# Optimization experiments

Hardware: AMD Instinct MI355X
Metric: run time of the kernel (lower is better)

Reference implementation:

```python
import jax, jax.numpy as jnp
import numpy as np

N_NODES = 100000
N_EDGES = 3200000
N_GRAPHS = 1024


def _glorot(key, shape):
    fan_in, fan_out = shape[0], shape[1]
    lim = jnp.sqrt(6.0 / (fan_in + fan_out))
    return jax.random.uniform(key, shape, minval=-lim, maxval=lim, dtype=jnp.float32)


def setup_inputs() -> dict:
    key = jax.random.key(0)
    ks = jax.random.split(key, 9)
    x = jax.random.normal(ks[0], (N_NODES, 3), dtype=jnp.float32)
    edge_index = jax.random.randint(ks[1], (2, N_EDGES), 0, N_NODES, dtype=jnp.int64)
    batch = jnp.sort(jax.random.randint(ks[2], (N_NODES,), 0, N_GRAPHS, dtype=jnp.int64))
    return {
        "x": x,
        "edge_index": edge_index,
        "batch": batch,
        "W1": _glorot(ks[3], (3, 16)),
        "b1": jnp.zeros((16,), jnp.float32),
        "W2": _glorot(ks[4], (16, 16)),
        "b2": jnp.zeros((16,), jnp.float32),
        "Wl": _glorot(ks[5], (16, 7)),
        "bl": jnp.zeros((7,), jnp.float32),
    }


def gcn_conv(x, edge_index, W, b, num_nodes):
    """GCNConv with normalize=True, add_self_loops=True (PyG defaults)."""
    x = x @ W  # linear transform first: [N, F_out]
    loop = jnp.arange(num_nodes, dtype=edge_index.dtype)
    row = jnp.concatenate([edge_index[0], loop])  # source nodes
    col = jnp.concatenate([edge_index[1], loop])  # target nodes
    # degree of target nodes (edge weight 1 incl. self loops)
    deg = jax.ops.segment_sum(jnp.ones_like(col, dtype=x.dtype), col,
                              num_segments=num_nodes)
    dinv = jnp.where(deg > 0, jax.lax.rsqrt(deg), 0.0)
    norm = dinv[row] * dinv[col]  # [E+N]
    msg = x[row] * norm[:, None]  # gather + normalize
    out = jax.ops.segment_sum(msg, col, num_segments=num_nodes)  # scatter-add
    return out + b


def reference(x, edge_index, batch, W1, b1, W2, b2, Wl, bl):
    h = jax.nn.relu(gcn_conv(x, edge_index, W1, b1, N_NODES))
    h = gcn_conv(h, edge_index, W2, b2, N_NODES)
    pooled = jax.ops.segment_sum(h, batch, num_segments=N_GRAPHS)  # global_add_pool
    logits = pooled @ Wl + bl  # [G, 7]
    return jax.nn.log_softmax(logits, axis=1)
```

## Files before the change

### kernel.cpp

```cpp
#include <hip/hip_runtime.h>
#include <hip/hip_fp16.h>
#include <math.h>

#define N_NODES  100000
#define N_EDGES  3200000
#define N_GRAPHS 1024
#define NB_NODE  391
#define NBUCK    391
#define CAP      8960
#define NPS      512
#define ECH      6250

__device__ inline unsigned pack2(float a, float b) {
    union { __half2 h; unsigned u; } c;
    c.h = __floats2half2_rn(a, b);
    return c.u;
}
__device__ inline float2 up2(unsigned u) {
    union { unsigned u; __half2 h; } c; c.u = u;
    return __half22float2(c.h);
}
__device__ inline void acc8(float* a, uint4 v) {
    float2 f;
    f = up2(v.x); a[0] += f.x; a[1] += f.y;
    f = up2(v.y); a[2] += f.x; a[3] += f.y;
    f = up2(v.z); a[4] += f.x; a[5] += f.y;
    f = up2(v.w); a[6] += f.x; a[7] += f.y;
}

__global__ void k_initcur(int* __restrict__ gcursor) {
    int t = blockIdx.x * blockDim.x + threadIdx.x;
    if (t < NBUCK) gcursor[t] = t * CAP;
}

__global__ void k_pair_scatter(const int* __restrict__ row, const int* __restrict__ col,
                               int* __restrict__ gcursor, int* __restrict__ pairbuf) {
    __shared__ int            sbuf[ECH];
    __shared__ unsigned short sbk[ECH];
    __shared__ int            lhist[NBUCK];
    __shared__ int            lcur[NBUCK];
    __shared__ int            wbase[NBUCK];
    int t = threadIdx.x;
    int e0 = blockIdx.x * ECH;
    int n = N_EDGES - e0; if (n > ECH) n = ECH;
    for (int j = t; j < NBUCK; j += 256) lhist[j] = 0;
    __syncthreads();
    for (int k = t; k < n; k += 256)
        atomicAdd(&lhist[col[e0 + k] >> 8], 1);
    __syncthreads();
    if (t < 64) {
        int carry = 0;
        for (int c0 = 0; c0 < NBUCK; c0 += 64) {
            int idx = c0 + t;
            int v = (idx < NBUCK) ? lhist[idx] : 0;
            int orig = v;
#pragma unroll
            for (int o = 1; o < 64; o <<= 1) {
                int u = __shfl_up(v, o, 64);
                if (t >= o) v += u;
            }
            if (idx < NBUCK) lcur[idx] = v - orig + carry;
            carry += __shfl(v, 63, 64);
        }
    }
    __syncthreads();
    for (int j = t; j < NBUCK; j += 256) {
        int c = lhist[j];
        int g = c ? atomicAdd(&gcursor[j], c) : 0;
        wbase[j] = g - lcur[j];
    }
    __syncthreads();
    for (int k = t; k < n; k += 256) {
        int e = e0 + k;
        int c = col[e];
        int bk = c >> 8;
        int pos = atomicAdd(&lcur[bk], 1);
        sbuf[pos] = row[e] | ((c & 255) << 17);
        sbk[pos] = (unsigned short)bk;
    }
    __syncthreads();
    for (int k = t; k < n; k += 256) {
        int bk = sbk[k];
        int pos = wbase[bk] + k;
        if (pos < (bk + 1) * CAP)
            pairbuf[pos] = sbuf[k];
    }
}

__global__ void k_finalize(const int* __restrict__ pairbuf, const int* __restrict__ gcursor,
                           int2* __restrict__ rowse, float* __restrict__ dinv,
                           int* __restrict__ csr) {
    __shared__ int slice[CAP];
    __shared__ int lcnt[256];
    __shared__ int ls[256];
    __shared__ int cur[256];
    int t = threadIdx.x, b = blockIdx.x;
    int base = b * CAP;
    int cnt_b = gcursor[b] - base;
    if (cnt_b > CAP) cnt_b = CAP;
    lcnt[t] = 0;
    for (int k = t; k < cnt_b; k += 256) slice[k] = pairbuf[base + k];
    __syncthreads();
    for (int k = t; k < cnt_b; k += 256)
        atomicAdd(&lcnt[(slice[k] >> 17) & 255], 1);
    __syncthreads();
    int myc = lcnt[t];
    ls[t] = myc;
    __syncthreads();
    for (int o = 1; o < 256; o <<= 1) {
        int v = (t >= o) ? ls[t - o] : 0;
        __syncthreads();
        ls[t] += v;
        __syncthreads();
    }
    int node0 = b << 8;
    int nn = N_NODES - node0; if (nn > 256) nn = 256;
    int st = base + ls[t] - myc;
    cur[t] = st;
    if (t < nn) {
        rowse[node0 + t] = make_int2(st, st + myc);
        dinv[node0 + t] = rsqrtf((float)(myc + 1));
    }
    __syncthreads();
    for (int k = t; k < cnt_b; k += 256) {
        int p = slice[k];
        int pos = atomicAdd(&cur[(p >> 17) & 255], 1);
        csr[pos] = p & 0x1FFFF;
    }
}

__global__ void k_xw1(const float* __restrict__ dinv, const float* __restrict__ x,
                      const float* __restrict__ W1, __half* __restrict__ bufA16) {
    int i = blockIdx.x * blockDim.x + threadIdx.x;
    if (i >= N_NODES) return;
    float d = dinv[i];
    float x0 = x[i * 3 + 0], x1 = x[i * 3 + 1], x2 = x[i * 3 + 2];
    float v[16];
#pragma unroll
    for (int j = 0; j < 16; j++)
        v[j] = (x0 * W1[j] + x1 * W1[16 + j] + x2 * W1[32 + j]) * d;
    uint4 u0 = { pack2(v[0], v[1]), pack2(v[2], v[3]), pack2(v[4], v[5]), pack2(v[6], v[7]) };
    uint4 u1 = { pack2(v[8], v[9]), pack2(v[10], v[11]), pack2(v[12], v[13]), pack2(v[14], v[15]) };
    uint4* p = (uint4*)(bufA16 + (long long)i * 16);
    p[0] = u0; p[1] = u1;
}

__global__ void k_gather(const uint4* __restrict__ src16, const int* __restrict__ csr,
                         const int2* __restrict__ rowse, const float* __restrict__ dinv,
                         float* __restrict__ dst) {
    int t = threadIdx.x;
    int node = blockIdx.x * 128 + (t >> 1);
    int h = t & 1;
    if (node >= N_NODES) return;
    int2 se = rowse[node];
    int s = se.x, e = se.y;
    float acc[8];
    {
        uint4 u = src16[node * 2 + h];
        float2 f;
        f = up2(u.x); acc[0] = f.x; acc[1] = f.y;
        f = up2(u.y); acc[2] = f.x; acc[3] = f.y;
        f = up2(u.z); acc[4] = f.x; acc[5] = f.y;
        f = up2(u.w); acc[6] = f.x; acc[7] = f.y;
    }
    int j = s;
    for (; j + 8 <= e; j += 8) {
        int i0 = csr[j],     i1 = csr[j + 1], i2 = csr[j + 2], i3 = csr[j + 3];
        int i4 = csr[j + 4], i5 = csr[j + 5], i6 = csr[j + 6], i7 = csr[j + 7];
        uint4 v0 = src16[i0 * 2 + h], v1 = src16[i1 * 2 + h];
        uint4 v2 = src16[i2 * 2 + h], v3 = src16[i3 * 2 + h];
        uint4 v4 = src16[i4 * 2 + h], v5 = src16[i5 * 2 + h];
        uint4 v6 = src16[i6 * 2 + h], v7 = src16[i7 * 2 + h];
        acc8(acc, v0); acc8(acc, v1); acc8(acc, v2); acc8(acc, v3);
        acc8(acc, v4); acc8(acc, v5); acc8(acc, v6); acc8(acc, v7);
    }
    for (; j < e; j++) {
        int si = csr[j];
        acc8(acc, src16[si * 2 + h]);
    }
    float d = dinv[node];
    float4 o0 = { acc[0] * d, acc[1] * d, acc[2] * d, acc[3] * d };
    float4 o1 = { acc[4] * d, acc[5] * d, acc[6] * d, acc[7] * d };
    float4* dp = (float4*)(dst + (long long)node * 16 + h * 8);
    dp[0] = o0; dp[1] = o1;
}

__global__ void k_layer2(const float* __restrict__ b1, const float* __restrict__ W2,
                         const float* __restrict__ dinv,
                         __half* __restrict__ bufA16, const float* __restrict__ bufB) {
    __shared__ float sW[256];
    __shared__ float sB[16];
    int tid = threadIdx.x;
    if (tid < 256) sW[tid] = W2[tid];
    if (tid < 16) sB[tid] = b1[tid];
    __syncthreads();
    int i = blockIdx.x * blockDim.x + tid;
    if (i >= N_NODES) return;
    float hbuf[16];
#pragma unroll
    for (int k = 0; k < 16; k++) {
        float v = bufB[i * 16 + k] + sB[k];
        hbuf[k] = v > 0.f ? v : 0.f;
    }
    float d = dinv[i];
    float v[16];
#pragma unroll
    for (int j = 0; j < 16; j++) {
        float acc = 0.f;
#pragma unroll
        for (int k = 0; k < 16; k++) acc += hbuf[k] * sW[k * 16 + j];
        v[j] = acc * d;
    }
    uint4 u0 = { pack2(v[0], v[1]), pack2(v[2], v[3]), pack2(v[4], v[5]), pack2(v[6], v[7]) };
    uint4 u1 = { pack2(v[8], v[9]), pack2(v[10], v[11]), pack2(v[12], v[13]), pack2(v[14], v[15]) };
    uint4* p = (uint4*)(bufA16 + (long long)i * 16);
    p[0] = u0; p[1] = u1;
}

__global__ void k_pool_head(const float* __restrict__ agg2, const int* __restrict__ batch,
                            const float* __restrict__ b2, const float* __restrict__ Wl,
                            const float* __restrict__ bl, float* __restrict__ out) {
    int g = blockIdx.x;
    int t = threadIdx.x;
    __shared__ int range[2];
    __shared__ float part[64];
    __shared__ float pooled[16];
    __shared__ float logits[7];
    if (t < 2) {
        int target = g + t;
        int lo = 0, hi = N_NODES;
        while (lo < hi) {
            int mid = (lo + hi) >> 1;
            if (batch[mid] < target) lo = mid + 1; else hi = mid;
        }
        range[t] = lo;
    }
    __syncthreads();
    int s = range[0], e = range[1];
    int f = t & 15, chunk = t >> 4;
    float acc = 0.f;
    for (int i = s + chunk; i < e; i += 4) acc += agg2[(long long)i * 16 + f];
    part[t] = acc;
    __syncthreads();
    if (t < 16) {
        float p = part[t] + part[t + 16] + part[t + 32] + part[t + 48];
        pooled[t] = p + (float)(e - s) * b2[t];
    }
    __syncthreads();
    if (t < 7) {
        float a = bl[t];
#pragma unroll
        for (int k = 0; k < 16; k++) a += pooled[k] * Wl[k * 7 + t];
        logits[t] = a;
    }
    __syncthreads();
    if (t == 0) {
        float m = logits[0];
#pragma unroll
        for (int c = 1; c < 7; c++) m = fmaxf(m, logits[c]);
        float sum = 0.f;
#pragma unroll
        for (int c = 0; c < 7; c++) sum += expf(logits[c] - m);
        float lse = logf(sum) + m;
#pragma unroll
        for (int c = 0; c < 7; c++) out[g * 7 + c] = logits[c] - lse;
    }
}

extern "C" void kernel_launch(void* const* d_in, const int* in_sizes, int n_in,
                              void* d_out, int out_size, void* d_ws, size_t ws_size,
                              hipStream_t stream) {
    const float* x     = (const float*)d_in[0];
    const int*   ei    = (const int*)d_in[1];
    const int*   batch = (const int*)d_in[2];
    const float* W1    = (const float*)d_in[3];
    const float* b1    = (const float*)d_in[4];
    const float* W2    = (const float*)d_in[5];
    const float* b2    = (const float*)d_in[6];
    const float* Wl    = (const float*)d_in[7];
    const float* bl    = (const float*)d_in[8];
    float* out = (float*)d_out;

    const int* row = ei;
    const int* col = ei + N_EDGES;

    int*    gcursor = (int*)d_ws;
    float*  dinv    = (float*)d_ws + 400;
    int2*   rowse   = (int2*)((int*)d_ws + 100400);
    int*    csr     = (int*)d_ws + 300400;
    int*    pairbuf = (int*)d_ws + 3803760;
    __half* bufA16  = (__half*)pairbuf;
    float*  bufB    = (float*)pairbuf + 800000;

    const int BT = 256;
    int gatherBlocks = (N_NODES + 127) / 128;

    k_initcur<<<2, BT, 0, stream>>>(gcursor);
    k_pair_scatter<<<NPS, BT, 0, stream>>>(row, col, gcursor, pairbuf);
    k_finalize<<<NBUCK, BT, 0, stream>>>(pairbuf, gcursor, rowse, dinv, csr);
    k_xw1<<<NB_NODE, BT, 0, stream>>>(dinv, x, W1, bufA16);
    k_gather<<<gatherBlocks, BT, 0, stream>>>((const uint4*)bufA16, csr, rowse, dinv, bufB);
    k_layer2<<<NB_NODE, BT, 0, stream>>>(b1, W2, dinv, bufA16, bufB);
    k_gather<<<gatherBlocks, BT, 0, stream>>>((const uint4*)bufA16, csr, rowse, dinv, bufB);
    k_pool_head<<<N_GRAPHS, 64, 0, stream>>>(bufB, batch, b2, Wl, bl, out);
}
```

Baseline: 233.2 us.

## Fuse XW1 into CSR finalize and layer-2 transform into first gather

The first-layer linear transform moves into the CSR finalize kernel, and the bias/ReLU/W2 transform moves into the first gather kernel through shared memory. This removes two launches and the fp32 intermediate round trip through global memory. The second gather now uses four threads per node with uint2 loads, and the CSR is written in place into the pair buffer. Cursor init becomes a memset, and the scatter uses more, smaller chunks without bounds checks. The fused gather adds a block-level sync and extra shared memory per block.

```diff
diff --git a/kernel.cpp b/kernel.cpp
--- a/kernel.cpp
+++ b/kernel.cpp
@@ -5,11 +5,10 @@
 #define N_NODES  100000
 #define N_EDGES  3200000
 #define N_GRAPHS 1024
-#define NB_NODE  391
 #define NBUCK    391
 #define CAP      8960
-#define NPS      512
-#define ECH      6250
+#define NPS      1024
+#define ECH      3125
 
 __device__ inline unsigned pack2(float a, float b) {
     union { __half2 h; unsigned u; } c;
@@ -27,10 +26,10 @@
     f = up2(v.z); a[4] += f.x; a[5] += f.y;
     f = up2(v.w); a[6] += f.x; a[7] += f.y;
 }
-
-__global__ void k_initcur(int* __restrict__ gcursor) {
-    int t = blockIdx.x * blockDim.x + threadIdx.x;
-    if (t < NBUCK) gcursor[t] = t * CAP;
+__device__ inline void acc4(float* a, uint2 v) {
+    float2 f;
+    f = up2(v.x); a[0] += f.x; a[1] += f.y;
+    f = up2(v.y); a[2] += f.x; a[3] += f.y;
 }
 
 __global__ void k_pair_scatter(const int* __restrict__ row, const int* __restrict__ col,
@@ -42,10 +41,9 @@
     __shared__ int            wbase[NBUCK];
     int t = threadIdx.x;
     int e0 = blockIdx.x * ECH;
-    int n = N_EDGES - e0; if (n > ECH) n = ECH;
     for (int j = t; j < NBUCK; j += 256) lhist[j] = 0;
     __syncthreads();
-    for (int k = t; k < n; k += 256)
+    for (int k = t; k < ECH; k += 256)
         atomicAdd(&lhist[col[e0 + k] >> 8], 1);
     __syncthreads();
     if (t < 64) {
@@ -67,10 +65,10 @@
     for (int j = t; j < NBUCK; j += 256) {
         int c = lhist[j];
         int g = c ? atomicAdd(&gcursor[j], c) : 0;
-        wbase[j] = g - lcur[j];
-    }
-    __syncthreads();
-    for (int k = t; k < n; k += 256) {
+        wbase[j] = j * CAP + g - lcur[j];
+    }
+    __syncthreads();
+    for (int k = t; k < ECH; k += 256) {
         int e = e0 + k;
         int c = col[e];
         int bk = c >> 8;
@@ -79,7 +77,7 @@
         sbk[pos] = (unsigned short)bk;
     }
     __syncthreads();
-    for (int k = t; k < n; k += 256) {
+    for (int k = t; k < ECH; k += 256) {
         int bk = sbk[k];
         int pos = wbase[bk] + k;
         if (pos < (bk + 1) * CAP)
@@ -87,18 +85,21 @@
     }
 }
 
-__global__ void k_finalize(const int* __restrict__ pairbuf, const int* __restrict__ gcursor,
+__global__ void k_finalize(int* __restrict__ pairbuf, const int* __restrict__ gcursor,
                            int2* __restrict__ rowse, float* __restrict__ dinv,
-                           int* __restrict__ csr) {
+                           const float* __restrict__ x, const float* __restrict__ W1,
+                           __half* __restrict__ bufA16) {
     __shared__ int slice[CAP];
     __shared__ int lcnt[256];
     __shared__ int ls[256];
     __shared__ int cur[256];
+    __shared__ float sw1[48];
     int t = threadIdx.x, b = blockIdx.x;
     int base = b * CAP;
-    int cnt_b = gcursor[b] - base;
+    int cnt_b = gcursor[b];
     if (cnt_b > CAP) cnt_b = CAP;
     lcnt[t] = 0;
+    if (t < 48) sw1[t] = W1[t];
     for (int k = t; k < cnt_b; k += 256) slice[k] = pairbuf[base + k];
     __syncthreads();
     for (int k = t; k < cnt_b; k += 256)
@@ -113,49 +114,48 @@
         ls[t] += v;
         __syncthreads();
     }
-    int node0 = b << 8;
-    int nn = N_NODES - node0; if (nn > 256) nn = 256;
+    int node = (b << 8) + t;
     int st = base + ls[t] - myc;
     cur[t] = st;
-    if (t < nn) {
-        rowse[node0 + t] = make_int2(st, st + myc);
-        dinv[node0 + t] = rsqrtf((float)(myc + 1));
+    if (node < N_NODES) {
+        rowse[node] = make_int2(st, st + myc);
+        float d = rsqrtf((float)(myc + 1));
+        dinv[node] = d;
+        float x0 = x[node * 3 + 0], x1 = x[node * 3 + 1], x2 = x[node * 3 + 2];
+        float v[16];
+#pragma unroll
+        for (int j = 0; j < 16; j++)
+            v[j] = (x0 * sw1[j] + x1 * sw1[16 + j] + x2 * sw1[32 + j]) * d;
+        uint4 u0 = { pack2(v[0], v[1]), pack2(v[2], v[3]), pack2(v[4], v[5]), pack2(v[6], v[7]) };
+        uint4 u1 = { pack2(v[8], v[9]), pack2(v[10], v[11]), pack2(v[12], v[13]), pack2(v[14], v[15]) };
+        uint4* p = (uint4*)(bufA16 + (long long)node * 16);
+        p[0] = u0; p[1] = u1;
     }
     __syncthreads();
     for (int k = t; k < cnt_b; k += 256) {
         int p = slice[k];
         int pos = atomicAdd(&cur[(p >> 17) & 255], 1);
-        csr[pos] = p & 0x1FFFF;
-    }
-}
-
-__global__ void k_xw1(const float* __restrict__ dinv, const float* __restrict__ x,
-                      const float* __restrict__ W1, __half* __restrict__ bufA16) {
-    int i = blockIdx.x * blockDim.x + threadIdx.x;
-    if (i >= N_NODES) return;
-    float d = dinv[i];
-    float x0 = x[i * 3 + 0], x1 = x[i * 3 + 1], x2 = x[i * 3 + 2];
-    float v[16];
-#pragma unroll
-    for (int j = 0; j < 16; j++)
-        v[j] = (x0 * W1[j] + x1 * W1[16 + j] + x2 * W1[32 + j]) * d;
-    uint4 u0 = { pack2(v[0], v[1]), pack2(v[2], v[3]), pack2(v[4], v[5]), pack2(v[6], v[7]) };
-    uint4 u1 = { pack2(v[8], v[9]), pack2(v[10], v[11]), pack2(v[12], v[13]), pack2(v[14], v[15]) };
-    uint4* p = (uint4*)(bufA16 + (long long)i * 16);
-    p[0] = u0; p[1] = u1;
-}
-
-__global__ void k_gather(const uint4* __restrict__ src16, const int* __restrict__ csr,
-                         const int2* __restrict__ rowse, const float* __restrict__ dinv,
-                         float* __restrict__ dst) {
+        pairbuf[pos] = p & 0x1FFFF;
+    }
+}
+
+__global__ void k_gather1(const uint4* __restrict__ src16, const int* __restrict__ csr,
+                          const int2* __restrict__ rowse, const float* __restrict__ dinv,
+                          const float* __restrict__ b1, const float* __restrict__ W2,
+                          __half* __restrict__ out16) {
+    __shared__ float sh[128][17];
+    __shared__ float sW[256];
+    __shared__ float sb1[16];
     int t = threadIdx.x;
-    int node = blockIdx.x * 128 + (t >> 1);
-    int h = t & 1;
-    if (node >= N_NODES) return;
-    int2 se = rowse[node];
+    sW[t] = W2[t];
+    if (t < 16) sb1[t] = b1[t];
+    int local = t >> 1, h = t & 1;
+    int node = blockIdx.x * 128 + local;
+    bool act = node < N_NODES;
+    int2 se = act ? rowse[node] : make_int2(0, 0);
     int s = se.x, e = se.y;
-    float acc[8];
-    {
+    float acc[8] = {0, 0, 0, 0, 0, 0, 0, 0};
+    if (act) {
         uint4 u = src16[node * 2 + h];
         float2 f;
         f = up2(u.x); acc[0] = f.x; acc[1] = f.y;
@@ -174,47 +174,60 @@
         acc8(acc, v0); acc8(acc, v1); acc8(acc, v2); acc8(acc, v3);
         acc8(acc, v4); acc8(acc, v5); acc8(acc, v6); acc8(acc, v7);
     }
-    for (; j < e; j++) {
-        int si = csr[j];
-        acc8(acc, src16[si * 2 + h]);
-    }
+    for (; j < e; j++) acc8(acc, src16[csr[j] * 2 + h]);
+    float d = act ? dinv[node] : 0.f;
+#pragma unroll
+    for (int k = 0; k < 8; k++) {
+        float v = acc[k] * d + sb1[h * 8 + k];
+        sh[local][h * 8 + k] = v > 0.f ? v : 0.f;
+    }
+    __syncthreads();
+    float v[8];
+#pragma unroll
+    for (int jj = 0; jj < 8; jj++) {
+        int jo = h * 8 + jj;
+        float a = 0.f;
+#pragma unroll
+        for (int k = 0; k < 16; k++) a += sh[local][k] * sW[k * 16 + jo];
+        v[jj] = a * d;
+    }
+    if (act) {
+        uint4 u = { pack2(v[0], v[1]), pack2(v[2], v[3]), pack2(v[4], v[5]), pack2(v[6], v[7]) };
+        ((uint4*)(out16 + (long long)node * 16 + h * 8))[0] = u;
+    }
+}
+
+__global__ void k_gather2(const uint2* __restrict__ src16, const int* __restrict__ csr,
+                          const int2* __restrict__ rowse, const float* __restrict__ dinv,
+                          float* __restrict__ dst) {
+    int t = threadIdx.x;
+    int node = blockIdx.x * 64 + (t >> 2);
+    int h = t & 3;
+    if (node >= N_NODES) return;
+    int2 se = rowse[node];
+    int s = se.x, e = se.y;
+    float acc[4];
+    {
+        uint2 u = src16[node * 4 + h];
+        float2 f;
+        f = up2(u.x); acc[0] = f.x; acc[1] = f.y;
+        f = up2(u.y); acc[2] = f.x; acc[3] = f.y;
+    }
+    int j = s;
+    for (; j + 8 <= e; j += 8) {
+        int i0 = csr[j],     i1 = csr[j + 1], i2 = csr[j + 2], i3 = csr[j + 3];
+        int i4 = csr[j + 4], i5 = csr[j + 5], i6 = csr[j + 6], i7 = csr[j + 7];
+        uint2 v0 = src16[i0 * 4 + h], v1 = src16[i1 * 4 + h];
+        uint2 v2 = src16[i2 * 4 + h], v3 = src16[i3 * 4 + h];
+        uint2 v4 = src16[i4 * 4 + h], v5 = src16[i5 * 4 + h];
+        uint2 v6 = src16[i6 * 4 + h], v7 = src16[i7 * 4 + h];
+        acc4(acc, v0); acc4(acc, v1); acc4(acc, v2); acc4(acc, v3);
+        acc4(acc, v4); acc4(acc, v5); acc4(acc, v6); acc4(acc, v7);
+    }
+    for (; j < e; j++) acc4(acc, src16[csr[j] * 4 + h]);
     float d = dinv[node];
-    float4 o0 = { acc[0] * d, acc[1] * d, acc[2] * d, acc[3] * d };
-    float4 o1 = { acc[4] * d, acc[5] * d, acc[6] * d, acc[7] * d };
-    float4* dp = (float4*)(dst + (long long)node * 16 + h * 8);
-    dp[0] = o0; dp[1] = o1;
-}
-
-__global__ void k_layer2(const float* __restrict__ b1, const float* __restrict__ W2,
-                         const float* __restrict__ dinv,
-                         __half* __restrict__ bufA16, const float* __restrict__ bufB) {
-    __shared__ float sW[256];
-    __shared__ float sB[16];
-    int tid = threadIdx.x;
-    if (tid < 256) sW[tid] = W2[tid];
-    if (tid < 16) sB[tid] = b1[tid];
-    __syncthreads();
-    int i = blockIdx.x * blockDim.x + tid;
-    if (i >= N_NODES) return;
-    float hbuf[16];
-#pragma unroll
-    for (int k = 0; k < 16; k++) {
-        float v = bufB[i * 16 + k] + sB[k];
-        hbuf[k] = v > 0.f ? v : 0.f;
-    }
-    float d = dinv[i];
-    float v[16];
-#pragma unroll
-    for (int j = 0; j < 16; j++) {
-        float acc = 0.f;
-#pragma unroll
-        for (int k = 0; k < 16; k++) acc += hbuf[k] * sW[k * 16 + j];
-        v[j] = acc * d;
-    }
-    uint4 u0 = { pack2(v[0], v[1]), pack2(v[2], v[3]), pack2(v[4], v[5]), pack2(v[6], v[7]) };
-    uint4 u1 = { pack2(v[8], v[9]), pack2(v[10], v[11]), pack2(v[12], v[13]), pack2(v[14], v[15]) };
-    uint4* p = (uint4*)(bufA16 + (long long)i * 16);
-    p[0] = u0; p[1] = u1;
+    float4 o = { acc[0] * d, acc[1] * d, acc[2] * d, acc[3] * d };
+    ((float4*)(dst + (long long)node * 16 + h * 4))[0] = o;
 }
 
 __global__ void k_pool_head(const float* __restrict__ agg2, const int* __restrict__ batch,
@@ -287,20 +300,19 @@
     int*    gcursor = (int*)d_ws;
     float*  dinv    = (float*)d_ws + 400;
     int2*   rowse   = (int2*)((int*)d_ws + 100400);
-    int*    csr     = (int*)d_ws + 300400;
-    int*    pairbuf = (int*)d_ws + 3803760;
-    __half* bufA16  = (__half*)pairbuf;
-    float*  bufB    = (float*)pairbuf + 800000;
+    int*    pairbuf = (int*)d_ws + 300400;
+    __half* bufA16  = (__half*)((int*)d_ws + 3803760);
+    __half* bufB16  = (__half*)((int*)d_ws + 4603760);
+    float*  bufB    = (float*)d_ws + 5403760;
 
     const int BT = 256;
-    int gatherBlocks = (N_NODES + 127) / 128;
-
-    k_initcur<<<2, BT, 0, stream>>>(gcursor);
+
+    hipMemsetAsync(gcursor, 0, 400 * sizeof(int), stream);
     k_pair_scatter<<<NPS, BT, 0, stream>>>(row, col, gcursor, pairbuf);
-    k_finalize<<<NBUCK, BT, 0, stream>>>(pairbuf, gcursor, rowse, dinv, csr);
-    k_xw1<<<NB_NODE, BT, 0, stream>>>(dinv, x, W1, bufA16);
-    k_gather<<<gatherBlocks, BT, 0, stream>>>((const uint4*)bufA16, csr, rowse, dinv, bufB);
-    k_layer2<<<NB_NODE, BT, 0, stream>>>(b1, W2, dinv, bufA16, bufB);
-    k_gather<<<gatherBlocks, BT, 0, stream>>>((const uint4*)bufA16, csr, rowse, dinv, bufB);
+    k_finalize<<<NBUCK, BT, 0, stream>>>(pairbuf, gcursor, rowse, dinv, x, W1, bufA16);
+    k_gather1<<<(N_NODES + 127) / 128, BT, 0, stream>>>((const uint4*)bufA16, pairbuf, rowse,
+                                                        dinv, b1, W2, bufB16);
+    k_gather2<<<(N_NODES + 63) / 64, BT, 0, stream>>>((const uint2*)bufB16, pairbuf, rowse,
+                                                      dinv, bufB);
     k_pool_head<<<N_GRAPHS, 64, 0, stream>>>(bufB, batch, b2, Wl, bl, out);
 }
```

After: 230.3 us. About the same (-1.3%).
